# Performance work log

Hardware: AMD Instinct MI355X
Metric: run time of the kernel (lower is better)

Reference implementation:

```python
import jax, jax.numpy as jnp
import numpy as np

B = 262144
NUM_CLASSES = 100
D = 128            # embedding_latent_dim and MLP width
VQ_DIM = 64        # vq_embedding_dim
VQ_K = 512         # vq_num_embeddings
A = 64             # action_dim
SQUISH = 1.0
COMMIT = 0.25


def _dense_params(key, fan_in, fan_out, scale=None):
    # he_uniform-like init; exact init distribution irrelevant for correctness baseline
    kw, kb = jax.random.split(key)
    lim = np.sqrt(6.0 / fan_in)
    W = jax.random.uniform(kw, (fan_in, fan_out), minval=-lim, maxval=lim, dtype=jnp.float32)
    b = jnp.zeros((fan_out,), dtype=jnp.float32)
    return W, b


def setup_inputs() -> dict:
    key = jax.random.key(0)
    ks = jax.random.split(key, 16)
    obs = jax.random.randint(ks[0], (B,), 0, NUM_CLASSES)
    embed = jax.random.normal(ks[1], (NUM_CLASSES, D), dtype=jnp.float32)
    W0, b0 = _dense_params(ks[2], D, D)
    W1, b1 = _dense_params(ks[3], D, D)
    W2, b2 = _dense_params(ks[4], D, D)
    Wp, bp = _dense_params(ks[5], D, VQ_DIM)
    lim = np.sqrt(3.0 / VQ_DIM)  # variance_scaling fan_in uniform
    vq_emb = jax.random.uniform(ks[6], (VQ_K, VQ_DIM), minval=-lim, maxval=lim, dtype=jnp.float32)
    Wa = 0.01 * jax.random.normal(ks[7], (VQ_DIM, A), dtype=jnp.float32)
    ba = jnp.zeros((A,), dtype=jnp.float32)
    Ws = 0.01 * jax.random.normal(ks[8], (VQ_DIM, A), dtype=jnp.float32)
    bs = jnp.zeros((A,), dtype=jnp.float32)
    Wc0, bc0 = _dense_params(ks[9], VQ_DIM, 128)
    Wc1, bc1 = _dense_params(ks[10], 128, 128)
    Wc2, bc2 = _dense_params(ks[11], 128, 32)
    Wc3, bc3 = _dense_params(ks[12], 32, 1)
    return dict(obs=obs, embed=embed, W0=W0, b0=b0, W1=W1, b1=b1, W2=W2, b2=b2,
                Wp=Wp, bp=bp, vq_emb=vq_emb, Wa=Wa, ba=ba, Ws=Ws, bs=bs,
                Wc0=Wc0, bc0=bc0, Wc1=Wc1, bc1=bc1, Wc2=Wc2, bc2=bc2, Wc3=Wc3, bc3=bc3)


def reference(obs, embed, W0, b0, W1, b1, W2, b2, Wp, bp, vq_emb,
              Wa, ba, Ws, bs, Wc0, bc0, Wc1, bc1, Wc2, bc2, Wc3, bc3):
    # class embedding lookup: [B, D]
    y = embed[obs]
    z = jax.nn.relu(y @ W0 + b0)
    z = jax.nn.relu(z @ W1 + b1)
    z = jax.nn.relu(z @ W2 + b2)
    z = z @ Wp + bp  # project to vq_embedding_dim: [B, 64]
    # --- VectorQuantizer ---
    # pairwise squared distances [B, K] via expansion trick
    dists = (jnp.sum(z * z, axis=1, keepdims=True)
             - 2.0 * (z @ vq_emb.T)
             + jnp.sum(vq_emb * vq_emb, axis=1)[None, :])
    encoding_indices = jnp.argmin(dists, axis=1)  # [B]
    quantized = vq_emb[encoding_indices]          # gather == onehot @ emb
    q_ste = z + jax.lax.stop_gradient(quantized - z)  # straight-through
    e_latent = jnp.mean((jax.lax.stop_gradient(q_ste) - z) ** 2)
    q_latent = jnp.mean((q_ste - jax.lax.stop_gradient(z)) ** 2)
    vq_loss = q_latent + COMMIT * e_latent
    # actor heads
    actor_mean = jax.nn.sigmoid(q_ste @ Wa + ba)
    scale_diag = jax.nn.sigmoid(q_ste @ Ws + bs) * SQUISH + 1e-8
    # critic stack
    c = jax.nn.sigmoid(q_ste @ Wc0 + bc0)
    c = jax.nn.sigmoid(c @ Wc1 + bc1)
    c = jax.nn.sigmoid(c @ Wc2 + bc2)
    critic = jnp.squeeze(c @ Wc3 + bc3, axis=-1)
    return actor_mean, scale_diag, critic, vq_loss, encoding_indices
```

## Files before the change

### kernel.cpp

```cpp
#include <hip/hip_runtime.h>
#include <hip/hip_bf16.h>
#include <math.h>

#define NCLS 100
#define DD   128
#define VQD  64
#define VQK  512

__device__ __forceinline__ float sigmoidf_(float x) { return 1.0f / (1.0f + expf(-x)); }

__global__ __launch_bounds__(128) void class_forward(
    const float* __restrict__ embed,
    const float* __restrict__ W0, const float* __restrict__ b0,
    const float* __restrict__ W1, const float* __restrict__ b1,
    const float* __restrict__ W2, const float* __restrict__ b2,
    const float* __restrict__ Wp, const float* __restrict__ bp,
    const float* __restrict__ vq,
    const float* __restrict__ Wa, const float* __restrict__ ba,
    const float* __restrict__ Ws, const float* __restrict__ bs,
    const float* __restrict__ Wc0, const float* __restrict__ bc0,
    const float* __restrict__ Wc1, const float* __restrict__ bc1,
    const float* __restrict__ Wc2, const float* __restrict__ bc2,
    const float* __restrict__ Wc3, const float* __restrict__ bc3,
    float* __restrict__ am_c, float* __restrict__ sd_c,
    float* __restrict__ cr_c, float* __restrict__ ms_c, int* __restrict__ id_c)
{
    __shared__ float ya[128], za[128], q64[64], qs[64], red[128];
    __shared__ int   redi[128];
    const int c = blockIdx.x;
    const int t = threadIdx.x;

    ya[t] = embed[c * DD + t];
    __syncthreads();

    float acc = b0[t];
    #pragma unroll 16
    for (int k = 0; k < 128; ++k) acc = fmaf(ya[k], W0[k * 128 + t], acc);
    za[t] = fmaxf(acc, 0.0f);
    __syncthreads();

    acc = b1[t];
    #pragma unroll 16
    for (int k = 0; k < 128; ++k) acc = fmaf(za[k], W1[k * 128 + t], acc);
    ya[t] = fmaxf(acc, 0.0f);
    __syncthreads();

    acc = b2[t];
    #pragma unroll 16
    for (int k = 0; k < 128; ++k) acc = fmaf(ya[k], W2[k * 128 + t], acc);
    za[t] = fmaxf(acc, 0.0f);
    __syncthreads();

    if (t < 64) {
        float a2 = bp[t];
        #pragma unroll 16
        for (int k = 0; k < 128; ++k) a2 = fmaf(za[k], Wp[k * 64 + t], a2);
        q64[t] = a2;
    }
    __syncthreads();

    if (t < 64) { red[t] = q64[t] * q64[t]; } else red[t] = 0.0f;
    __syncthreads();
    for (int s = 64; s > 0; s >>= 1) { if (t < s) red[t] += red[t + s]; __syncthreads(); }
    const float zz = red[0];
    __syncthreads();

    float bestv = 3.4e38f;
    int   besti = 0;
    for (int cc = t; cc < VQK; cc += 128) {
        const float* e = vq + cc * VQD;
        float dot = 0.0f, esq = 0.0f;
        #pragma unroll 16
        for (int k = 0; k < VQD; ++k) {
            float ev = e[k];
            dot = fmaf(q64[k], ev, dot);
            esq = fmaf(ev, ev, esq);
        }
        float d = (zz - 2.0f * dot) + esq;
        if (d < bestv) { bestv = d; besti = cc; }
    }
    red[t] = bestv; redi[t] = besti;
    __syncthreads();
    for (int s = 64; s > 0; s >>= 1) {
        if (t < s) {
            float v = red[t + s]; int i2 = redi[t + s];
            if (v < red[t] || (v == red[t] && i2 < redi[t])) { red[t] = v; redi[t] = i2; }
        }
        __syncthreads();
    }
    const int best = redi[0];
    __syncthreads();

    if (t < 64) {
        float z  = q64[t];
        float qq = vq[best * VQD + t];
        float q_ste = z + (qq - z);
        qs[t] = q_ste;
        float dd = q_ste - z;
        red[t] = dd * dd;
    } else red[t] = 0.0f;
    __syncthreads();
    for (int s = 64; s > 0; s >>= 1) { if (t < s) red[t] += red[t + s]; __syncthreads(); }
    if (t == 0) { ms_c[c] = red[0]; id_c[c] = best; }

    {
        const int j = t & 63;
        const float* W = (t < 64) ? Wa : Ws;
        float a2 = (t < 64) ? ba[j] : bs[j];
        #pragma unroll 16
        for (int k = 0; k < 64; ++k) a2 = fmaf(qs[k], W[k * 64 + j], a2);
        float s = sigmoidf_(a2);
        if (t < 64) am_c[c * 64 + j] = s;
        else        sd_c[c * 64 + j] = s * 1.0f + 1e-8f;
    }

    acc = bc0[t];
    #pragma unroll 16
    for (int k = 0; k < 64; ++k) acc = fmaf(qs[k], Wc0[k * 128 + t], acc);
    ya[t] = sigmoidf_(acc);
    __syncthreads();

    acc = bc1[t];
    #pragma unroll 16
    for (int k = 0; k < 128; ++k) acc = fmaf(ya[k], Wc1[k * 128 + t], acc);
    za[t] = sigmoidf_(acc);
    __syncthreads();

    if (t < 32) {
        float a2 = bc2[t];
        #pragma unroll 16
        for (int k = 0; k < 128; ++k) a2 = fmaf(za[k], Wc2[k * 32 + t], a2);
        q64[t] = sigmoidf_(a2);
    }
    __syncthreads();

    if (t == 0) {
        float a2 = bc3[0];
        for (int k = 0; k < 32; ++k) a2 = fmaf(q64[k], Wc3[k], a2);
        cr_c[c] = a2;
    }
}

__global__ __launch_bounds__(256) void scatter_vec(
    const int* __restrict__ obs,
    const float4* __restrict__ amc, const float4* __restrict__ sdc,
    const float* __restrict__ crc,  const int* __restrict__ idc,
    float4* __restrict__ out_am, float4* __restrict__ out_sd,
    float* __restrict__ out_cr,  float* __restrict__ out_idx, int n4)
{
    const int e4 = blockIdx.x * 256 + threadIdx.x;
    if (e4 >= n4) return;
    const int i  = e4 >> 4;
    const int d4 = e4 & 15;
    const int c  = obs[i];
    const int off = (c << 4) + d4;
    out_am[e4] = amc[off];
    out_sd[e4] = sdc[off];
    if (d4 == 0) {
        out_cr[i]  = crc[c];
        out_idx[i] = (float)idc[c];
    }
}

__global__ __launch_bounds__(256) void hist_obs(
    const int* __restrict__ obs, unsigned int* __restrict__ counts, int n)
{
    __shared__ unsigned int h[NCLS];
    const int t = threadIdx.x;
    if (t < NCLS) h[t] = 0u;
    __syncthreads();
    for (int i = blockIdx.x * blockDim.x + t; i < n; i += gridDim.x * blockDim.x)
        atomicAdd(&h[obs[i]], 1u);
    __syncthreads();
    if (t < NCLS) atomicAdd(&counts[t], h[t]);
}

__global__ __launch_bounds__(128) void finalize_vq(
    const unsigned int* __restrict__ counts, const float* __restrict__ ms,
    float* __restrict__ out, int n)
{
    __shared__ double sd[128];
    const int t = threadIdx.x;
    double a = 0.0;
    if (t < NCLS) a = (double)counts[t] * (double)ms[t];
    sd[t] = a;
    __syncthreads();
    for (int s = 64; s > 0; s >>= 1) { if (t < s) sd[t] += sd[t + s]; __syncthreads(); }
    if (t == 0) out[0] = (float)(1.25 * sd[0] / ((double)n * 64.0));
}

extern "C" void kernel_launch(void* const* d_in, const int* in_sizes, int n_in,
                              void* d_out, int out_size, void* d_ws, size_t ws_size,
                              hipStream_t stream)
{
    const int*   obs   = (const int*)d_in[0];
    const float* embed = (const float*)d_in[1];
    const float* W0  = (const float*)d_in[2];   const float* b0  = (const float*)d_in[3];
    const float* W1  = (const float*)d_in[4];   const float* b1  = (const float*)d_in[5];
    const float* W2  = (const float*)d_in[6];   const float* b2  = (const float*)d_in[7];
    const float* Wp  = (const float*)d_in[8];   const float* bp  = (const float*)d_in[9];
    const float* vq  = (const float*)d_in[10];
    const float* Wa  = (const float*)d_in[11];  const float* ba  = (const float*)d_in[12];
    const float* Ws  = (const float*)d_in[13];  const float* bs  = (const float*)d_in[14];
    const float* Wc0 = (const float*)d_in[15];  const float* bc0 = (const float*)d_in[16];
    const float* Wc1 = (const float*)d_in[17];  const float* bc1 = (const float*)d_in[18];
    const float* Wc2 = (const float*)d_in[19];  const float* bc2 = (const float*)d_in[20];
    const float* Wc3 = (const float*)d_in[21];  const float* bc3 = (const float*)d_in[22];

    const int n = in_sizes[0];

    float* ws_f  = (float*)d_ws;
    float* am_c  = ws_f;
    float* sd_c  = am_c + NCLS * 64;
    float* cr_c  = sd_c + NCLS * 64;
    float* ms_c  = cr_c + NCLS;
    int*   id_c  = (int*)(ms_c + NCLS);
    unsigned int* counts = (unsigned int*)(id_c + NCLS);

    float* out     = (float*)d_out;
    float* out_am  = out;
    float* out_sd  = out + (size_t)n * 64;
    float* out_cr  = out + (size_t)n * 128;
    float* out_vq  = out_cr + n;
    float* out_idx = out_vq + 1;

    hipMemsetAsync(counts, 0, NCLS * sizeof(unsigned int), stream);

    class_forward<<<NCLS, 128, 0, stream>>>(
        embed, W0, b0, W1, b1, W2, b2, Wp, bp, vq,
        Wa, ba, Ws, bs, Wc0, bc0, Wc1, bc1, Wc2, bc2, Wc3, bc3,
        am_c, sd_c, cr_c, ms_c, id_c);

    const int n4 = n * 16;
    scatter_vec<<<(n4 + 255) / 256, 256, 0, stream>>>(
        obs, (const float4*)am_c, (const float4*)sd_c, cr_c, id_c,
        (float4*)out_am, (float4*)out_sd, out_cr, out_idx, n4);

    hist_obs<<<512, 256, 0, stream>>>(obs, counts, n);

    finalize_vq<<<1, 128, 0, stream>>>(counts, ms_c, out_vq, n);
}
```

Measured before the change: 255.2 us.

## Fuse histogram and VQ-loss finalize into scatter kernel with last-block reduction

Removes the memset, the histogram kernel and the finalize kernel. Each scatter block now reduces its per-row VQ squared-error contributions in shared memory, atomically adds the sum to a global double accumulator, and the last block (found with a ticket counter) writes the loss. Output stores become nontemporal to avoid polluting cache. This saves two kernel launches and one extra pass over obs, at the cost of a shared-memory reduction in every one of the ~16K blocks plus a global atomic per block.

```diff
diff --git a/kernel.cpp b/kernel.cpp
--- a/kernel.cpp
+++ b/kernel.cpp
@@ -6,6 +6,8 @@
 #define DD   128
 #define VQD  64
 #define VQK  512
+
+typedef float f32x4 __attribute__((ext_vector_type(4)));
 
 __device__ __forceinline__ float sigmoidf_(float x) { return 1.0f / (1.0f + expf(-x)); }
 
@@ -23,12 +25,15 @@
     const float* __restrict__ Wc2, const float* __restrict__ bc2,
     const float* __restrict__ Wc3, const float* __restrict__ bc3,
     float* __restrict__ am_c, float* __restrict__ sd_c,
-    float* __restrict__ cr_c, float* __restrict__ ms_c, int* __restrict__ id_c)
+    float* __restrict__ cr_c, float* __restrict__ ms_c, int* __restrict__ id_c,
+    double* __restrict__ vq_acc, unsigned int* __restrict__ ticket)
 {
     __shared__ float ya[128], za[128], q64[64], qs[64], red[128];
     __shared__ int   redi[128];
     const int c = blockIdx.x;
     const int t = threadIdx.x;
+
+    if (c == 0 && t == 0) { *vq_acc = 0.0; *ticket = 0u; }
 
     ya[t] = embed[c * DD + t];
     __syncthreads();
@@ -141,52 +146,46 @@
     }
 }
 
-__global__ __launch_bounds__(256) void scatter_vec(
+__global__ __launch_bounds__(256) void scatter_fused(
     const int* __restrict__ obs,
-    const float4* __restrict__ amc, const float4* __restrict__ sdc,
+    const f32x4* __restrict__ amc, const f32x4* __restrict__ sdc,
     const float* __restrict__ crc,  const int* __restrict__ idc,
-    float4* __restrict__ out_am, float4* __restrict__ out_sd,
-    float* __restrict__ out_cr,  float* __restrict__ out_idx, int n4)
+    const float* __restrict__ msc,
+    f32x4* __restrict__ out_am, f32x4* __restrict__ out_sd,
+    float* __restrict__ out_cr,  float* __restrict__ out_idx,
+    float* __restrict__ out_vq,
+    double* __restrict__ vq_acc, unsigned int* __restrict__ ticket,
+    int n4, int n, unsigned int nblocks)
 {
-    const int e4 = blockIdx.x * 256 + threadIdx.x;
-    if (e4 >= n4) return;
-    const int i  = e4 >> 4;
-    const int d4 = e4 & 15;
-    const int c  = obs[i];
-    const int off = (c << 4) + d4;
-    out_am[e4] = amc[off];
-    out_sd[e4] = sdc[off];
-    if (d4 == 0) {
-        out_cr[i]  = crc[c];
-        out_idx[i] = (float)idc[c];
-    }
-}
-
-__global__ __launch_bounds__(256) void hist_obs(
-    const int* __restrict__ obs, unsigned int* __restrict__ counts, int n)
-{
-    __shared__ unsigned int h[NCLS];
-    const int t = threadIdx.x;
-    if (t < NCLS) h[t] = 0u;
-    __syncthreads();
-    for (int i = blockIdx.x * blockDim.x + t; i < n; i += gridDim.x * blockDim.x)
-        atomicAdd(&h[obs[i]], 1u);
-    __syncthreads();
-    if (t < NCLS) atomicAdd(&counts[t], h[t]);
-}
-
-__global__ __launch_bounds__(128) void finalize_vq(
-    const unsigned int* __restrict__ counts, const float* __restrict__ ms,
-    float* __restrict__ out, int n)
-{
-    __shared__ double sd[128];
-    const int t = threadIdx.x;
-    double a = 0.0;
-    if (t < NCLS) a = (double)counts[t] * (double)ms[t];
-    sd[t] = a;
-    __syncthreads();
-    for (int s = 64; s > 0; s >>= 1) { if (t < s) sd[t] += sd[t + s]; __syncthreads(); }
-    if (t == 0) out[0] = (float)(1.25 * sd[0] / ((double)n * 64.0));
+    __shared__ double sd[256];
+    const int t  = threadIdx.x;
+    const int e4 = blockIdx.x * 256 + t;
+    double contrib = 0.0;
+    if (e4 < n4) {
+        const int i  = e4 >> 4;
+        const int d4 = e4 & 15;
+        const int c  = obs[i];
+        const int off = (c << 4) + d4;
+        __builtin_nontemporal_store(amc[off], out_am + e4);
+        __builtin_nontemporal_store(sdc[off], out_sd + e4);
+        if (d4 == 0) {
+            __builtin_nontemporal_store(crc[c], out_cr + i);
+            __builtin_nontemporal_store((float)idc[c], out_idx + i);
+            contrib = (double)msc[c];
+        }
+    }
+    sd[t] = contrib;
+    __syncthreads();
+    for (int s = 128; s > 0; s >>= 1) { if (t < s) sd[t] += sd[t + s]; __syncthreads(); }
+    if (t == 0) {
+        atomicAdd(vq_acc, sd[0]);
+        __threadfence();
+        const unsigned int old = atomicAdd(ticket, 1u);
+        if (old == nblocks - 1u) {
+            const double s = atomicAdd(vq_acc, 0.0);
+            out_vq[0] = (float)(1.25 * s / ((double)n * 64.0));
+        }
+    }
 }
 
 extern "C" void kernel_launch(void* const* d_in, const int* in_sizes, int n_in,
@@ -209,13 +208,14 @@
 
     const int n = in_sizes[0];
 
-    float* ws_f  = (float*)d_ws;
+    double* vq_acc = (double*)d_ws;
+    unsigned int* ticket = (unsigned int*)(vq_acc + 1);
+    float* ws_f  = (float*)(ticket + 2);
     float* am_c  = ws_f;
     float* sd_c  = am_c + NCLS * 64;
     float* cr_c  = sd_c + NCLS * 64;
     float* ms_c  = cr_c + NCLS;
     int*   id_c  = (int*)(ms_c + NCLS);
-    unsigned int* counts = (unsigned int*)(id_c + NCLS);
 
     float* out     = (float*)d_out;
     float* out_am  = out;
@@ -224,19 +224,15 @@
     float* out_vq  = out_cr + n;
     float* out_idx = out_vq + 1;
 
-    hipMemsetAsync(counts, 0, NCLS * sizeof(unsigned int), stream);
-
     class_forward<<<NCLS, 128, 0, stream>>>(
         embed, W0, b0, W1, b1, W2, b2, Wp, bp, vq,
         Wa, ba, Ws, bs, Wc0, bc0, Wc1, bc1, Wc2, bc2, Wc3, bc3,
-        am_c, sd_c, cr_c, ms_c, id_c);
+        am_c, sd_c, cr_c, ms_c, id_c, vq_acc, ticket);
 
     const int n4 = n * 16;
-    scatter_vec<<<(n4 + 255) / 256, 256, 0, stream>>>(
-        obs, (const float4*)am_c, (const float4*)sd_c, cr_c, id_c,
-        (float4*)out_am, (float4*)out_sd, out_cr, out_idx, n4);
-
-    hist_obs<<<512, 256, 0, stream>>>(obs, counts, n);
-
-    finalize_vq<<<1, 128, 0, stream>>>(counts, ms_c, out_vq, n);
+    const unsigned int nblocks = (unsigned int)((n4 + 255) / 256);
+    scatter_fused<<<nblocks, 256, 0, stream>>>(
+        obs, (const f32x4*)am_c, (const f32x4*)sd_c, cr_c, id_c, ms_c,
+        (f32x4*)out_am, (f32x4*)out_sd, out_cr, out_idx, out_vq,
+        vq_acc, ticket, n4, n, nblocks);
 }
```

Result: slower. 849.9 us (+233.0%).
